# Kernel optimization log

Hardware: AMD Instinct MI355X
Metric: run time of the kernel (lower is better)

The kernel has to match this reference:

```python
import jax, jax.numpy as jnp
import numpy as np

N = 4096

def setup_inputs() -> dict:
    key = jax.random.key(0)
    kA, kB = jax.random.split(key)
    A = jnp.tril(jax.random.normal(kA, (N, N), dtype=jnp.float32))
    B = jnp.tril(jax.random.normal(kB, (N, N), dtype=jnp.float32))
    return {"A": A, "B": B}

def reference(A, B):
    # Product of two lower-triangular matrices; result is lower-triangular.
    # tril applied to the dense matmul reproduces the intended math exactly
    # (and zeroes any numerical noise in the structural-zero upper triangle).
    return jnp.tril(jnp.matmul(A, B))
```

## Files before the change

kernel.cpp:

```cpp
#include <hip/hip_runtime.h>
#include <stdint.h>

#define NN 4096
#define NB2 16
#define BK 64

#define NUNITS 260
#define ZBASE 260
#define TGRID 380
#define NSPLIT 78
#define NWSLOTS 202

#define PGRID_W 8192
#define PGRID_A 8504

typedef __bf16 bf16x8 __attribute__((ext_vector_type(8)));
typedef float f32x4 __attribute__((ext_vector_type(4)));
typedef unsigned short ushort8 __attribute__((ext_vector_type(8)));

__device__ __forceinline__ unsigned short f2bf(float x) {
    union { float f; unsigned int u; } v; v.f = x;
    unsigned int u = v.u;
    u += 0x7fffu + ((u >> 16) & 1u);
    return (unsigned short)(u >> 16);
}

#define GLOAD16(g, l) __builtin_amdgcn_global_load_lds( \
    (const __attribute__((address_space(1))) unsigned int*)(g), \
    (__attribute__((address_space(3))) unsigned int*)(l), 16, 0, 0)

__device__ __forceinline__ void split_decode(int z, int& bi, int& bj, int& nu, int& u0) {
    int d = 15, acc = 0;
    for (;;) {
        nu = (d + 4) >> 2;
        int cnt = NB2 - d;
        if (z < cnt) { bj = z; bi = z + d; u0 = acc + z * nu; return; }
        z -= cnt; acc += cnt * nu; --d;
    }
}

__global__ __launch_bounds__(256) void prep(const float* __restrict__ A,
                                            const float* __restrict__ B,
                                            unsigned short* __restrict__ Ab,
                                            unsigned short* __restrict__ Bt,
                                            float* __restrict__ C) {
    __shared__ float tile[64][65];
    int bid = blockIdx.x;
    int tid = threadIdx.x;

    if (bid < 4096) {
        int i = bid;
        int nslots = ((i >> 8) + 1) * 32;
        const float4* src = reinterpret_cast<const float4*>(A + (size_t)i * NN);
        unsigned short* dst = Ab + (size_t)i * NN;
        for (int p = tid; p < nslots; p += 256) {
            float4 x0 = src[p * 2], x1 = src[p * 2 + 1];
            ushort8 o;
            o[0] = f2bf(x0.x); o[1] = f2bf(x0.y); o[2] = f2bf(x0.z); o[3] = f2bf(x0.w);
            o[4] = f2bf(x1.x); o[5] = f2bf(x1.y); o[6] = f2bf(x1.z); o[7] = f2bf(x1.w);
            *reinterpret_cast<ushort8*>(dst + p * 8) = o;
        }
        return;
    }
    if (bid < 8192) {
        int s = bid - 4096;
        int n64 = s >> 6, k64 = s & 63;
        if (k64 < (n64 & ~3)) return;
        int n0 = n64 * 64, k0 = k64 * 64;
        int tx = tid & 63, ty = tid >> 6;
#pragma unroll
        for (int r = 0; r < 16; ++r) {
            int k = ty + r * 4;
            tile[k][tx] = B[(size_t)(k0 + k) * NN + n0 + tx];
        }
        __syncthreads();
#pragma unroll
        for (int r = 0; r < 16; ++r) {
            int n = ty + r * 4;
            Bt[(size_t)(n0 + n) * NN + k0 + tx] = f2bf(tile[tx][n]);
        }
        return;
    }
    {
        int z = bid - 8192;
        int bi, bj, nu, u0; split_decode(z >> 2, bi, bj, nu, u0);
        int part = z & 3;
        float4 zf = make_float4(0.f, 0.f, 0.f, 0.f);
        float4* cp = reinterpret_cast<float4*>(C + (size_t)(bi * 256 + part * 64) * NN + (size_t)bj * 256);
#pragma unroll
        for (int i2 = 0; i2 < 16; ++i2) {
            int slot = tid + i2 * 256;
            int row = slot >> 6, c4 = slot & 63;
            cp[(size_t)row * (NN / 4) + c4] = zf;
        }
    }
}

__global__ __launch_bounds__(512, 1) void trimm(const unsigned short* __restrict__ Ab,
                                                const unsigned short* __restrict__ Bt,
                                                float* __restrict__ C,
                                                float* __restrict__ W,
                                                int useW) {
    int bid = blockIdx.x;
    int tid = threadIdx.x;
    int lane = tid & 63;
    int w = tid >> 6;

    if (bid >= ZBASE) {
        int r = bid - ZBASE, bi = 0;
        while (r >= NB2 - 1 - bi) { r -= NB2 - 1 - bi; ++bi; }
        int bj = bi + 1 + r;
        float4 z = make_float4(0.f, 0.f, 0.f, 0.f);
        float4* cp = reinterpret_cast<float4*>(C + (size_t)bi * 256 * NN + (size_t)bj * 256);
#pragma unroll
        for (int i2 = 0; i2 < 32; ++i2) {
            int slot = tid + i2 * 512;
            int row = slot >> 6, c4 = slot & 63;
            cp[(size_t)row * (NN / 4) + c4] = z;
        }
        return;
    }

    int bi, bj, k_lo, nt;
    bool atom;
    {
        int r = bid, d = 15, nu;
        for (;;) {
            nu = (d + 4) >> 2;
            int cnt = (NB2 - d) * nu;
            if (r < cnt) break;
            r -= cnt; --d;
        }
        int t = r / nu, part = r - t * nu;
        bj = t; bi = t + d;
        atom = (nu > 1);
        int ntk = 4 * (d + 1);
        int ntb = ntk / nu, rem = ntk % nu;
        nt = ntb + (part < rem ? 1 : 0);
        int skip = part * ntb + (part < rem ? part : rem);
        k_lo = bj * 256 + skip * BK;
    }

    __shared__ unsigned short As[4][128 * 64];
    __shared__ unsigned short Bs[4][128 * 64];

    int wr = w >> 2;
    int wc = w & 3;
    int hb = wc >> 1;
    int colb = (wc & 1) * 64;
    int fr = lane & 15;
    int c0 = (((lane >> 4) ^ (lane & 7)) * 8);
    int c1 = ((((lane >> 4) | 4) ^ (lane & 7)) * 8);

    int srow = tid >> 3;
    int schunk = ((tid & 7) ^ (srow & 7)) * 8;
    const unsigned short* gA = Ab + (size_t)(bi * 256 + srow) * NN + schunk;
    const unsigned short* gB = Bt + (size_t)(bj * 256 + srow) * NN + schunk;

    f32x4 acc[8][4];
#pragma unroll
    for (int m = 0; m < 8; ++m)
#pragma unroll
        for (int n = 0; n < 4; ++n)
            acc[m][n] = (f32x4){0.f, 0.f, 0.f, 0.f};

    bf16x8 aX[4], aY[4], bv0[4], bv1[4];

#define STG(XS, gX, h, slot, kk) do { \
        unsigned short* d_ = &XS[slot][0] + tid * 8; \
        GLOAD16(gX + (size_t)(h) * 128 * NN + (kk), d_); \
        GLOAD16(gX + (size_t)((h) * 128 + 64) * NN + (kk), d_ + 4096); \
    } while (0)

#define RDA(Ap, G, CC, AV) do { \
        _Pragma("unroll") for (int m_ = 0; m_ < 4; ++m_) { \
            int r_ = (((G) * 4 + m_) * 16 + fr) * 64; \
            AV[m_] = *reinterpret_cast<const bf16x8*>(&Ap[r_ + (CC)]); \
        } \
    } while (0)

#define RDB(Bp, CC, BV) do { \
        _Pragma("unroll") for (int n_ = 0; n_ < 4; ++n_) { \
            int r_ = (colb + n_ * 16 + fr) * 64; \
            BV[n_] = *reinterpret_cast<const bf16x8*>(&Bp[r_ + (CC)]); \
        } \
    } while (0)

#define MFMA16(AV, BV, MB) do { \
        _Pragma("unroll") for (int m_ = 0; m_ < 4; ++m_) \
        _Pragma("unroll") for (int n_ = 0; n_ < 4; ++n_) \
            acc[(MB) + m_][n_] = __builtin_amdgcn_mfma_f32_16x16x32_bf16(AV[m_], BV[n_], acc[(MB) + m_][n_], 0, 0, 0); \
    } while (0)

#define PRIO1 __builtin_amdgcn_s_setprio(1)
#define PRIO0 __builtin_amdgcn_s_setprio(0)

    STG(As, gA, 0, 0, k_lo);
    STG(Bs, gB, 0, 0, k_lo);
    STG(Bs, gB, 1, 1, k_lo);
    STG(As, gA, 1, 1, k_lo);

    for (int t = 0; t < nt; ++t) {
        __syncthreads();

        const unsigned short* Ac = &As[(2 * t + wr) & 3][0];
        const unsigned short* Bc = &Bs[(2 * t + hb) & 3][0];
        int np0 = (2 * t + 2) & 3, np1 = (2 * t + 3) & 3;
        int kkn = (t + 1 < nt) ? (k_lo + (t + 1) * BK) : k_lo;

        RDA(Ac, 0, c0, aX);
        RDB(Bc, c0, bv0);
        RDA(Ac, 1, c0, aY);
        STG(As, gA, 0, np0, kkn);
        STG(Bs, gB, 0, np0, kkn);
        PRIO1; MFMA16(aX, bv0, 0); PRIO0;
        RDA(Ac, 0, c1, aX);
        RDB(Bc, c1, bv1);
        STG(Bs, gB, 1, np1, kkn);
        STG(As, gA, 1, np1, kkn);
        PRIO1; MFMA16(aY, bv0, 4); PRIO0;
        RDA(Ac, 1, c1, aY);
        PRIO1; MFMA16(aX, bv1, 0); PRIO0;
        PRIO1; MFMA16(aY, bv1, 4); PRIO0;
    }
    asm volatile("s_waitcnt vmcnt(0)" ::: "memory");
#undef STG
#undef RDA
#undef RDB
#undef MFMA16
#undef PRIO1
#undef PRIO0

    int r4 = (lane >> 4) * 4;
    if (atom && useW) {
        float* wb = W + (size_t)bid * 65536;
#pragma unroll
        for (int m = 0; m < 8; ++m)
#pragma unroll
            for (int n = 0; n < 4; ++n) {
                int row = wr * 128 + m * 16 + r4;
                int col = wc * 64 + n * 16 + fr;
                float* wp = wb + (size_t)row * 256 + col;
#pragma unroll
                for (int r2 = 0; r2 < 4; ++r2)
                    wp[(size_t)r2 * 256] = acc[m][n][r2];
            }
    } else if (atom) {
#pragma unroll
        for (int m = 0; m < 8; ++m)
#pragma unroll
            for (int n = 0; n < 4; ++n) {
                int row = bi * 256 + wr * 128 + m * 16 + r4;
                int col = bj * 256 + wc * 64 + n * 16 + fr;
                float* cp = C + (size_t)row * NN + col;
#pragma unroll
                for (int r2 = 0; r2 < 4; ++r2)
                    atomicAdd(&cp[(size_t)r2 * NN], acc[m][n][r2]);
            }
    } else {
#pragma unroll
        for (int m = 0; m < 8; ++m)
#pragma unroll
            for (int n = 0; n < 4; ++n) {
                int row = bi * 256 + wr * 128 + m * 16 + r4;
                int col = bj * 256 + wc * 64 + n * 16 + fr;
                float* cp = C + (size_t)row * NN + col;
#pragma unroll
                for (int r2 = 0; r2 < 4; ++r2)
                    cp[(size_t)r2 * NN] = acc[m][n][r2];
            }
    }
}

__global__ __launch_bounds__(256) void merge(const float* __restrict__ W,
                                             float* __restrict__ C) {
    int blk = blockIdx.x;
    int z = blk >> 3;
    int sub = blk & 7;
    int tid = threadIdx.x;
    int bi, bj, nu, u0; split_decode(z, bi, bj, nu, u0);
    const float4* w0 = reinterpret_cast<const float4*>(W + (size_t)u0 * 65536) + sub * 2048;
#pragma unroll 2
    for (int it = 0; it < 8; ++it) {
        int s = tid + it * 256;
        int row = s >> 6, c4 = s & 63;
        float4 a = w0[s];
        for (int p = 1; p < nu; ++p) {
            float4 b = w0[(size_t)p * 16384 + s];
            a.x += b.x; a.y += b.y; a.z += b.z; a.w += b.w;
        }
        float4* cp = reinterpret_cast<float4*>(C) +
                     (size_t)(bi * 256 + sub * 32 + row) * (NN / 4) + bj * 64 + c4;
        *cp = a;
    }
}

extern "C" void kernel_launch(void* const* d_in, const int* in_sizes, int n_in,
                              void* d_out, int out_size, void* d_ws, size_t ws_size,
                              hipStream_t stream) {
    const float* A = (const float*)d_in[0];
    const float* B = (const float*)d_in[1];
    float* C = (float*)d_out;
    unsigned short* Ab = (unsigned short*)d_ws;
    unsigned short* Bt = Ab + (size_t)NN * NN;
    const size_t base = (size_t)2 * NN * NN * sizeof(unsigned short);
    const size_t wbytes = (size_t)NWSLOTS * 65536 * sizeof(float);
    const int useW = (ws_size >= base + wbytes) ? 1 : 0;
    float* W = (float*)((char*)d_ws + base);

    prep<<<useW ? PGRID_W : PGRID_A, 256, 0, stream>>>(A, B, Ab, Bt, C);
    trimm<<<TGRID, 512, 0, stream>>>(Ab, Bt, C, W, useW);
    if (useW) merge<<<NSPLIT * 8, 256, 0, stream>>>(W, C);
}
```

Measured before the change: 79.47 us.

## Remap block IDs to pair heavy and light row-blocks across XCDs

Changes the mapping from block index to work unit so that bid&7 (the XCD index under round-robin dispatch) selects a pair of row-blocks (15-x and x), balancing the total work per XCD and keeping a row's A tiles on one XCD's L2. Zero-fill blocks are interleaved into the leftover slots of each XCD's share. Workspace slots are recomputed through split_decode so the reduction pass still finds partial sums. This adds index-decode arithmetic per block, and it depends on the hardware dispatching blocks round-robin across 8 XCDs.

```diff
diff --git a/kernel.cpp b/kernel.cpp
--- a/kernel.cpp
+++ b/kernel.cpp
@@ -5,8 +5,6 @@
 #define NB2 16
 #define BK 64
 
-#define NUNITS 260
-#define ZBASE 260
 #define TGRID 380
 #define NSPLIT 78
 #define NWSLOTS 202
@@ -28,6 +26,11 @@
 #define GLOAD16(g, l) __builtin_amdgcn_global_load_lds( \
     (const __attribute__((address_space(1))) unsigned int*)(g), \
     (__attribute__((address_space(3))) unsigned int*)(l), 16, 0, 0)
+
+__device__ __forceinline__ int row_units(int bi) {
+    int n = bi + 1, q = n >> 2, r = n & 3;
+    return 2 * q * (q + 1) + r * (q + 1);
+}
 
 __device__ __forceinline__ void split_decode(int z, int& bi, int& bj, int& nu, int& u0) {
     int d = 15, acc = 0;
@@ -106,39 +109,62 @@
     int lane = tid & 63;
     int w = tid >> 6;
 
-    if (bid >= ZBASE) {
-        int r = bid - ZBASE, bi = 0;
-        while (r >= NB2 - 1 - bi) { r -= NB2 - 1 - bi; ++bi; }
-        int bj = bi + 1 + r;
-        float4 z = make_float4(0.f, 0.f, 0.f, 0.f);
-        float4* cp = reinterpret_cast<float4*>(C + (size_t)bi * 256 * NN + (size_t)bj * 256);
-#pragma unroll
-        for (int i2 = 0; i2 < 32; ++i2) {
-            int slot = tid + i2 * 512;
-            int row = slot >> 6, c4 = slot & 63;
-            cp[(size_t)row * (NN / 4) + c4] = z;
-        }
-        return;
-    }
-
-    int bi, bj, k_lo, nt;
-    bool atom;
+    int bi = 0, bj = 0, k_lo = 0, nt = 0, wslot = 0;
+    bool atom = false;
     {
-        int r = bid, d = 15, nu;
-        for (;;) {
-            nu = (d + 4) >> 2;
-            int cnt = (NB2 - d) * nu;
-            if (r < cnt) break;
-            r -= cnt; --d;
-        }
-        int t = r / nu, part = r - t * nu;
-        bj = t; bi = t + d;
-        atom = (nu > 1);
-        int ntk = 4 * (d + 1);
-        int ntb = ntk / nu, rem = ntk % nu;
-        nt = ntb + (part < rem ? 1 : 0);
-        int skip = part * ntb + (part < rem ? part : rem);
-        k_lo = bj * 256 + skip * BK;
+        bool zero = false;
+        int zi = 0;
+        if (bid >= 328) {
+            zero = true; zi = 68 + (bid - 328);
+        } else {
+            int x = bid & 7, s = bid >> 3;
+            int rA = 15 - x, rB = x;
+            int uA = row_units(rA), uB = row_units(rB);
+            if (s >= uA + uB) {
+                int sb = 0;
+                for (int y = 0; y < x; ++y)
+                    sb += 41 - (row_units(15 - y) + row_units(y));
+                zero = true; zi = sb + (s - uA - uB);
+            } else {
+                int row, idx;
+                if (s < uA) { row = rA; idx = s; }
+                else        { row = rB; idx = s - uA; }
+                bi = row;
+                int d, nu;
+                for (bj = 0;; ++bj) {
+                    d = bi - bj;
+                    nu = (d + 4) >> 2;
+                    if (idx < nu) break;
+                    idx -= nu;
+                }
+                int part = idx;
+                atom = (nu > 1);
+                int ntk = 4 * (d + 1);
+                int ntb = ntk / nu, rem = ntk % nu;
+                nt = ntb + (part < rem ? 1 : 0);
+                int skip = part * ntb + (part < rem ? part : rem);
+                k_lo = bj * 256 + skip * BK;
+                if (atom) {
+                    int z = (15 - d) * (16 - d) / 2 + bj;
+                    int tb, tj, tn, u0; split_decode(z, tb, tj, tn, u0);
+                    wslot = u0 + part;
+                }
+            }
+        }
+        if (zero) {
+            int r = zi, zbi = 0;
+            while (r >= NB2 - 1 - zbi) { r -= NB2 - 1 - zbi; ++zbi; }
+            int zbj = zbi + 1 + r;
+            float4 z4 = make_float4(0.f, 0.f, 0.f, 0.f);
+            float4* cp = reinterpret_cast<float4*>(C + (size_t)zbi * 256 * NN + (size_t)zbj * 256);
+#pragma unroll
+            for (int i2 = 0; i2 < 32; ++i2) {
+                int slot = tid + i2 * 512;
+                int row = slot >> 6, c4 = slot & 63;
+                cp[(size_t)row * (NN / 4) + c4] = z4;
+            }
+            return;
+        }
     }
 
     __shared__ unsigned short As[4][128 * 64];
@@ -233,7 +259,7 @@
 
     int r4 = (lane >> 4) * 4;
     if (atom && useW) {
-        float* wb = W + (size_t)bid * 65536;
+        float* wb = W + (size_t)wslot * 65536;
 #pragma unroll
         for (int m = 0; m < 8; ++m)
 #pragma unroll
```

Result: slower. 95.78 us (+20.5%).
